# Performance work log

Measured on AMD Instinct MI355X. Metric: run time of the kernel, lower is better.

Reference implementation:

```python
import jax, jax.numpy as jnp
import numpy as np

AMPLITUDE_STD = 4.2  # repo constant (unexported); normalization scale for ln_mag
EPS = 1e-8


def _interp_bias(table, x):
    # Linear interpolation of a 1D table over frequency domain [-1, 1].
    n = table.shape[0]
    idx = jnp.clip((x + 1.0) * 0.5 * (n - 1), 0.0, float(n - 1))
    i0 = jnp.floor(idx).astype(jnp.int32)
    i1 = jnp.minimum(i0 + 1, n - 1)
    w = idx - i0.astype(idx.dtype)
    return table[i0] * (1.0 - w) + table[i1] * w


def setup_inputs() -> dict:
    key = jax.random.key(0)
    k1, k2, k3, k4 = jax.random.split(key, 4)
    B, F, P, W, H = 8, 128, 32, 96, 96
    return {
        "mode_shapes": jax.random.normal(k1, (B, 2, P, W, H), dtype=jnp.float32),
        "mode_responses": jax.random.normal(k2, (B, F, 2, P), dtype=jnp.float32),
        "freqs": jax.random.uniform(k3, (B, F), dtype=jnp.float32, minval=-1.0, maxval=1.0),
        "bias_table": jax.random.normal(k4, (250,), dtype=jnp.float32) * 0.1,
    }


def reference(mode_shapes, mode_responses, freqs, bias_table):
    B, _, P, W, H = mode_shapes.shape
    F = mode_responses.shape[1]
    # _normalize_mode: L2 norm over (real/imag, W, H) per (batch, peak)
    norm = jnp.sqrt(jnp.sum(mode_shapes ** 2, axis=(1, 3, 4)))  # (B,P)
    ms = mode_shapes / (norm[:, None, :, None, None] + EPS)
    s_r, s_i = ms[:, 0], ms[:, 1]                                # (B,P,W,H)
    t_r, t_i = mode_responses[:, :, 0], mode_responses[:, :, 1]  # (B,F,P)
    f = 1.0 / P
    # complex superposition over modes: contraction over n_peaks
    rr = jnp.einsum('bpwh,bfp->bfwh', s_r, t_r)
    ii = jnp.einsum('bpwh,bfp->bfwh', s_i, t_i)
    ri = jnp.einsum('bpwh,bfp->bfwh', s_r, t_i)
    ir = jnp.einsum('bpwh,bfp->bfwh', s_i, t_r)
    r_new = f * (rr - ii)  # (B,F,W,H)
    i_new = f * (ri + ir)
    mag2 = r_new ** 2 + i_new ** 2
    bias = _interp_bias(bias_table, freqs)                       # (B,F)
    ln_mag = (jnp.log(mag2 + EPS) + bias[:, :, None, None]) / AMPLITUDE_STD
    fnorm = jnp.sum(mag2, axis=(-1, -2), keepdims=True)
    fnorm = jnp.sqrt(jnp.clip(fnorm, jnp.finfo(fnorm.dtype).eps))
    normed_field = jnp.stack([r_new / fnorm, i_new / fnorm], axis=2)  # (B,F,2,W,H)
    # aux sparsity loss over mode responses
    mr = mode_responses.reshape(B, F * 2, P)
    aux_sparse = jnp.mean(jnp.mean(jnp.log(jnp.linalg.norm(mr, axis=1) + 1.0), axis=1))
    return ln_mag, normed_field, aux_sparse
```

## Files before the change

### kernel.cpp

```cpp
#include <hip/hip_runtime.h>
#include <math.h>

#define WHN 9216
#define PN 32
#define FN 128
#define BN 8
#define EPSF 1e-8f
#define INV_STD 0.23809523809f
#define AUX_IDX 28311552

typedef __attribute__((ext_vector_type(8))) short short8;
typedef __attribute__((ext_vector_type(16))) float f32x16;

__device__ __forceinline__ unsigned short f2bf(float x) {
  unsigned int u = __float_as_uint(x);
  unsigned int r = (u + 0x7FFFu + ((u >> 16) & 1u)) >> 16;
  return (unsigned short)r;
}
__device__ __forceinline__ float bf2f(unsigned short h) {
  return __uint_as_float(((unsigned int)h) << 16);
}

__global__ __launch_bounds__(256) void k_gram(const float* __restrict__ ms,
                                              float* __restrict__ wsM,
                                              float* __restrict__ wsA,
                                              float* __restrict__ part,
                                              int use_part) {
  const int b = blockIdx.y;
  const int chunk = blockIdx.x;
  const int tid = threadIdx.x;
  __shared__ float4 sA[32][32];
  __shared__ float4 sB[32][32];
  __shared__ float pbuf[2][2048];
  const float4* ms4 = (const float4*)ms;
#pragma unroll
  for (int k = 0; k < 4; ++k) {
    int i4 = tid + k * 256;
    int xq = i4 & 31, p = i4 >> 5;
    sA[xq][p ^ xq] = ms4[((b * 2 + 0) * 32 + p) * 2304 + chunk * 32 + xq];
    sB[xq][p ^ xq] = ms4[((b * 2 + 1) * 32 + p) * 2304 + chunk * 32 + xq];
  }
  __syncthreads();
  const int w = tid >> 6, lane = tid & 63;
  const int pg = lane & 7, qg = lane >> 3;
  float accM[4][4] = {{0}}, accA[4][4] = {{0}};
  for (int xq = w; xq < 32; xq += 4) {
    float4 pa[4], pb[4], qa[4], qb[4];
#pragma unroll
    for (int j = 0; j < 4; ++j) {
      pa[j] = sA[xq][(pg + 8 * j) ^ xq];
      pb[j] = sB[xq][(pg + 8 * j) ^ xq];
      qa[j] = sA[xq][(qg + 8 * j) ^ xq];
      qb[j] = sB[xq][(qg + 8 * j) ^ xq];
    }
#pragma unroll
    for (int j = 0; j < 4; ++j)
#pragma unroll
      for (int k = 0; k < 4; ++k) {
        accM[j][k] += pa[j].x * qa[k].x + pb[j].x * qb[k].x
                    + pa[j].y * qa[k].y + pb[j].y * qb[k].y
                    + pa[j].z * qa[k].z + pb[j].z * qb[k].z
                    + pa[j].w * qa[k].w + pb[j].w * qb[k].w;
        accA[j][k] += pa[j].x * qb[k].x - pb[j].x * qa[k].x
                    + pa[j].y * qb[k].y - pb[j].y * qa[k].y
                    + pa[j].z * qb[k].z - pb[j].z * qa[k].z
                    + pa[j].w * qb[k].w - pb[j].w * qa[k].w;
      }
  }
  if (w < 2) {
#pragma unroll
    for (int j = 0; j < 4; ++j)
#pragma unroll
      for (int k = 0; k < 4; ++k) {
        pbuf[w][lane * 32 + j * 4 + k] = accM[j][k];
        pbuf[w][lane * 32 + 16 + j * 4 + k] = accA[j][k];
      }
  }
  __syncthreads();
  if (w >= 2) {
#pragma unroll
    for (int j = 0; j < 4; ++j)
#pragma unroll
      for (int k = 0; k < 4; ++k) {
        pbuf[w - 2][lane * 32 + j * 4 + k] += accM[j][k];
        pbuf[w - 2][lane * 32 + 16 + j * 4 + k] += accA[j][k];
      }
  }
  __syncthreads();
  for (int idx = tid; idx < 2048; idx += 256) {
    float v = pbuf[0][idx] + pbuf[1][idx];
    if (use_part) {
      part[((size_t)(b * 72 + chunk)) * 2048 + idx] = v;
    } else {
      int lane2 = idx >> 5, r = idx & 31;
      int mat = r >> 4, rr = r & 15, j = rr >> 2, k = rr & 3;
      int p = (lane2 & 7) + 8 * j, q = (lane2 >> 3) + 8 * k;
      float* dst = mat ? wsA : wsM;
      atomicAdd(dst + (b << 10) + p * 32 + q, v);
    }
  }
}

__global__ __launch_bounds__(256) void k_mid(const float* __restrict__ part,
                                             float* __restrict__ wsM,
                                             float* __restrict__ wsA,
                                             float* __restrict__ wsc,
                                             float* __restrict__ out) {
  int g = blockIdx.x * 256 + threadIdx.x;
  if (g == 0) out[AUX_IDX] = 0.f;
  int b = g >> 11, idx = g & 2047;
  const float* p = part + ((size_t)b * 72) * 2048 + idx;
  float s = 0.f;
#pragma unroll 8
  for (int c = 0; c < 72; ++c) s += p[(size_t)c * 2048];
  int lane2 = idx >> 5, r = idx & 31;
  int mat = r >> 4, rr = r & 15, j = rr >> 2, k = rr & 3;
  int pp = (lane2 & 7) + 8 * j, q = (lane2 >> 3) + 8 * k;
  (mat ? wsA : wsM)[(b << 10) + pp * 32 + q] = s;
  if (!mat && pp == q) wsc[(b << 5) + pp] = (1.0f / 32.0f) / (sqrtf(s) + EPSF);
}

__global__ void k_cfromM(const float* __restrict__ wsM, float* __restrict__ wsc,
                         float* __restrict__ out) {
  int tid = threadIdx.x;
  if (tid == 0) out[AUX_IDX] = 0.f;
  int b = tid >> 5, p = tid & 31;
  float m = wsM[(b << 10) + p * 33];
  wsc[tid] = (1.0f / 32.0f) / (sqrtf(m) + EPSF);
}

__global__ __launch_bounds__(64) void k_fnb(const float* __restrict__ t,
                                            const float* __restrict__ freqs,
                                            const float* __restrict__ btab,
                                            const float* __restrict__ wsM,
                                            const float* __restrict__ wsA,
                                            const float* __restrict__ wsc,
                                            float* __restrict__ wsinv,
                                            float* __restrict__ wsbias,
                                            float* __restrict__ out) {
  const int lane = threadIdx.x;
  if (blockIdx.x >= 1024) {
    const int b = blockIdx.x - 1024;
    const int p = lane & 31, comp = lane >> 5;
    float acc = 0.f;
#pragma unroll 4
    for (int f = 0; f < FN; ++f) {
      float v = t[((size_t)(b * FN + f) * 2 + comp) * PN + p];
      acc = fmaf(v, v, acc);
    }
    acc += __shfl_xor(acc, 32);
    float val = logf(sqrtf(acc) + 1.0f);
#pragma unroll
    for (int off = 1; off <= 16; off <<= 1) val += __shfl_xor(val, off);
    if (lane == 0) atomicAdd(out + AUX_IDX, val * (1.0f / 256.0f));
    return;
  }
  const int bf = blockIdx.x;
  const int b = bf >> 7;
  __shared__ float tt[64];
  {
    int p = lane & 31, comp = lane >> 5;
    tt[lane] = t[(bf * 2 + comp) * PN + p] * wsc[(b << 5) + p];
  }
  __syncthreads();
  const int pp = lane & 31, qh = lane >> 5;
  const float* Mrow = wsM + (b << 10) + pp * 32 + qh * 16;
  const float* Arow = wsA + (b << 10) + pp * 32 + qh * 16;
  float ap = tt[pp], bp = tt[32 + pp];
  float S = 0.f;
#pragma unroll
  for (int k = 0; k < 16; ++k) {
    int q = qh * 16 + k;
    float aq = tt[q], bq = tt[32 + q];
    S += (ap * aq + bp * bq) * Mrow[k] + 2.0f * (bp * aq) * Arow[k];
  }
#pragma unroll
  for (int off = 32; off; off >>= 1) S += __shfl_xor(S, off);
  if (lane == 0) {
    float fn = sqrtf(fmaxf(S, 1.1920929e-7f));
    wsinv[bf] = 1.0f / fn;
    float x = freqs[bf];
    float idx = (x + 1.0f) * 0.5f * 249.0f;
    idx = fminf(fmaxf(idx, 0.0f), 249.0f);
    float fi = floorf(idx);
    int i0 = (int)fi;
    int i1 = min(i0 + 1, 249);
    float wvv = idx - fi;
    wsbias[bf] = btab[i0] * (1.0f - wvv) + btab[i1] * wvv;
  }
}

#define MFMA32(A, B, C) __builtin_amdgcn_mfma_f32_32x32x16_bf16(A, B, C, 0, 0, 0)
__global__ __launch_bounds__(256) void k_main(const float* __restrict__ ms,
                                              const float* __restrict__ t,
                                              const float* __restrict__ wsc,
                                              const float* __restrict__ wsinv,
                                              const float* __restrict__ wsbias,
                                              float* __restrict__ out) {
  __shared__ short tHs[4096];
  __shared__ short tLs[4096];
  __shared__ float sInv[64], sBias[64], sC[32];
  const int b = blockIdx.y;
  const int tid = threadIdx.x;
  const int lane = tid & 63, wv = tid >> 6;
  const int col = lane & 31, hf = lane >> 5;
  const int pix = blockIdx.x * 128 + wv * 32 + col;
  const int f0 = blockIdx.z * 64;

  const float* msb = ms + (size_t)b * 64 * WHN + pix;
  short8 sHf[4], sLf[4];
#pragma unroll
  for (int kg = 0; kg < 4; ++kg) {
#pragma unroll
    for (int j = 0; j < 8; ++j) {
      int k = kg * 16 + hf * 8 + j;
      float v = msb[(size_t)k * WHN];
      unsigned short h = f2bf(v);
      sHf[kg][j] = (short)h;
      sLf[kg][j] = (short)f2bf(v - bf2f(h));
    }
  }
  short8 msk;
#pragma unroll
  for (int j = 0; j < 8; ++j) msk[j] = (short)0x8000;
  short8 nH2 = sHf[2] ^ msk, nL2 = sLf[2] ^ msk;
  short8 nH3 = sHf[3] ^ msk, nL3 = sLf[3] ^ msk;

  if (tid < 64) sInv[tid] = wsinv[b * 128 + f0 + tid];
  else if (tid < 128) sBias[tid - 64] = wsbias[b * 128 + f0 + (tid - 64)];
  if (tid >= 224) sC[tid - 224] = wsc[b * 32 + (tid - 224)];
  __syncthreads();

#pragma unroll
  for (int it = 0; it < 2; ++it) {
    int gidx = tid + it * 256;
    int fl = gidx >> 3, g = gidx & 7;
    const float* src = t + ((size_t)(b * 128 + f0 + fl) * 2 + (g >> 2)) * 32 + (g & 3) * 8;
    int gs = g ^ (fl & 7);
    short8 hv, lv;
#pragma unroll
    for (int e = 0; e < 8; ++e) {
      float v = src[e] * sC[(g & 3) * 8 + e];
      unsigned short h = f2bf(v);
      hv[e] = (short)h;
      lv[e] = (short)f2bf(v - bf2f(h));
    }
    *(short8*)&tHs[fl * 64 + gs * 8] = hv;
    *(short8*)&tLs[fl * 64 + gs * 8] = lv;
  }
  __syncthreads();

  float* outF = out + (size_t)BN * FN * WHN;

#pragma unroll
  for (int ft = 0; ft < 2; ++ft) {
    short8 tHf[4], tLf[4];
    int fl = ft * 32 + col;
    int fx = fl & 7;
#pragma unroll
    for (int kg = 0; kg < 4; ++kg) {
      int gs = (2 * kg + hf) ^ fx;
      tHf[kg] = *(const short8*)&tHs[fl * 64 + gs * 8];
      tLf[kg] = *(const short8*)&tLs[fl * 64 + gs * 8];
    }
    f32x16 aR, aI;
#pragma unroll
    for (int i = 0; i < 16; ++i) { aR[i] = 0.f; aI[i] = 0.f; }
    aR = MFMA32(tHf[0], sHf[0], aR); aR = MFMA32(tHf[0], sLf[0], aR); aR = MFMA32(tLf[0], sHf[0], aR);
    aR = MFMA32(tHf[1], sHf[1], aR); aR = MFMA32(tHf[1], sLf[1], aR); aR = MFMA32(tLf[1], sHf[1], aR);
    aR = MFMA32(tHf[2], nH2,    aR); aR = MFMA32(tHf[2], nL2,    aR); aR = MFMA32(tLf[2], nH2,    aR);
    aR = MFMA32(tHf[3], nH3,    aR); aR = MFMA32(tHf[3], nL3,    aR); aR = MFMA32(tLf[3], nH3,    aR);
    aI = MFMA32(tHf[0], sHf[2], aI); aI = MFMA32(tHf[0], sLf[2], aI); aI = MFMA32(tLf[0], sHf[2], aI);
    aI = MFMA32(tHf[1], sHf[3], aI); aI = MFMA32(tHf[1], sLf[3], aI); aI = MFMA32(tLf[1], sHf[3], aI);
    aI = MFMA32(tHf[2], sHf[0], aI); aI = MFMA32(tHf[2], sLf[0], aI); aI = MFMA32(tLf[2], sHf[0], aI);
    aI = MFMA32(tHf[3], sHf[1], aI); aI = MFMA32(tHf[3], sLf[1], aI); aI = MFMA32(tLf[3], sHf[1], aI);
#pragma unroll
    for (int r = 0; r < 16; ++r) {
      int row = (r & 3) + 8 * (r >> 2) + 4 * hf;
      int fo = ft * 32 + row;
      float vr = aR[r], vi = aI[r];
      float mag2 = fmaf(vr, vr, vi * vi);
      float ln = (__logf(mag2 + EPSF) + sBias[fo]) * INV_STD;
      float inv = sInv[fo];
      size_t fg = (size_t)(b * 128 + f0 + fo);
      __builtin_nontemporal_store(ln, out + fg * WHN + pix);
      __builtin_nontemporal_store(vr * inv, outF + (fg * 2) * WHN + pix);
      __builtin_nontemporal_store(vi * inv, outF + (fg * 2 + 1) * WHN + pix);
    }
  }
}

extern "C" void kernel_launch(void* const* d_in, const int* in_sizes, int n_in,
                              void* d_out, int out_size, void* d_ws, size_t ws_size,
                              hipStream_t stream) {
  const float* ms = (const float*)d_in[0];
  const float* t  = (const float*)d_in[1];
  const float* fr = (const float*)d_in[2];
  const float* bt = (const float*)d_in[3];
  float* out = (float*)d_out;
  float* ws = (float*)d_ws;
  float* wsM = ws;
  float* wsA = ws + 8192;
  float* wsc = ws + 16384;
  float* wsinv = ws + 16640;
  float* wsbias = ws + 17664;
  float* part = ws + 18688;
  size_t need = ((size_t)18688 + (size_t)576 * 2048) * 4;
  int use_part = (ws_size >= need) ? 1 : 0;

  if (use_part) {
    hipLaunchKernelGGL(k_gram, dim3(72, 8), dim3(256), 0, stream, ms, wsM, wsA, part, 1);
    hipLaunchKernelGGL(k_mid, dim3(64), dim3(256), 0, stream, part, wsM, wsA, wsc, out);
  } else {
    hipMemsetAsync(ws, 0, 16384 * sizeof(float), stream);
    hipLaunchKernelGGL(k_gram, dim3(72, 8), dim3(256), 0, stream, ms, wsM, wsA, part, 0);
    hipLaunchKernelGGL(k_cfromM, dim3(1), dim3(256), 0, stream, wsM, wsc, out);
  }
  hipLaunchKernelGGL(k_fnb, dim3(1032), dim3(64), 0, stream, t, fr, bt, wsM, wsA, wsc, wsinv, wsbias, out);
  hipLaunchKernelGGL(k_main, dim3(72, 8, 2), dim3(256), 0, stream, ms, t, wsc, wsinv, wsbias, out);
}
```

Before: 171.6 us.

## Precompute split-bf16 mode-response tiles once and DMA them into LDS

The scaled, swizzled hi/lo bf16 split of the mode responses was recomputed by every k_main block (72x redundancy per batch/f-tile). Extra blocks in k_fnb now compute it once per batch into a workspace buffer. k_main loads it straight into LDS with global_load_lds, which removes per-block conversion work and one barrier. k_main also gains a min-blocks launch bound of 2 and uses the library bf16 conversion. The risks are extra workspace traffic and register pressure from the tighter launch bound.

```diff
diff --git a/kernel.cpp b/kernel.cpp
--- a/kernel.cpp
+++ b/kernel.cpp
@@ -1,4 +1,5 @@
 #include <hip/hip_runtime.h>
+#include <hip/hip_bf16.h>
 #include <math.h>
 
 #define WHN 9216
@@ -12,13 +13,16 @@
 typedef __attribute__((ext_vector_type(8))) short short8;
 typedef __attribute__((ext_vector_type(16))) float f32x16;
 
-__device__ __forceinline__ unsigned short f2bf(float x) {
-  unsigned int u = __float_as_uint(x);
-  unsigned int r = (u + 0x7FFFu + ((u >> 16) & 1u)) >> 16;
-  return (unsigned short)r;
-}
-__device__ __forceinline__ float bf2f(unsigned short h) {
-  return __uint_as_float(((unsigned int)h) << 16);
+__device__ __forceinline__ unsigned short bfbits(__hip_bfloat16 h) {
+  return *reinterpret_cast<unsigned short*>(&h);
+}
+
+__device__ __forceinline__ unsigned int bfsplit_pk(float v) {
+  __hip_bfloat16 h = __float2bfloat16(v);
+  unsigned int hs = bfbits(h);
+  float r = v - __bfloat162float(h);
+  unsigned int ls = bfbits(__float2bfloat16(r));
+  return hs | (ls << 16);
 }
 
 __global__ __launch_bounds__(256) void k_gram(const float* __restrict__ ms,
@@ -137,8 +141,34 @@
                                             const float* __restrict__ wsc,
                                             float* __restrict__ wsinv,
                                             float* __restrict__ wsbias,
+                                            short* __restrict__ wsT,
                                             float* __restrict__ out) {
   const int lane = threadIdx.x;
+  if (blockIdx.x >= 1032) {
+    const int b = blockIdx.x - 1032;
+    __shared__ float sc[32];
+    if (lane < 32) sc[lane] = wsc[b * 32 + lane];
+    __syncthreads();
+    short* dstH = wsT + (size_t)b * 16384;
+    short* dstL = dstH + 8192;
+#pragma unroll 2
+    for (int it = 0; it < 16; ++it) {
+      int slot = it * 64 + lane;
+      int fl = slot >> 3, g = slot & 7;
+      const float* src = t + ((size_t)(b * 128 + fl) * 2 + (g >> 2)) * 32 + (g & 3) * 8;
+      int gs = g ^ (fl & 7);
+      short8 hv, lv;
+#pragma unroll
+      for (int e = 0; e < 8; ++e) {
+        unsigned int pk = bfsplit_pk(src[e] * sc[(g & 3) * 8 + e]);
+        hv[e] = (short)(pk & 0xFFFFu);
+        lv[e] = (short)(pk >> 16);
+      }
+      *(short8*)&dstH[fl * 64 + gs * 8] = hv;
+      *(short8*)&dstL[fl * 64 + gs * 8] = lv;
+    }
+    return;
+  }
   if (blockIdx.x >= 1024) {
     const int b = blockIdx.x - 1024;
     const int p = lane & 31, comp = lane >> 5;
@@ -191,21 +221,36 @@
 }
 
 #define MFMA32(A, B, C) __builtin_amdgcn_mfma_f32_32x32x16_bf16(A, B, C, 0, 0, 0)
-__global__ __launch_bounds__(256) void k_main(const float* __restrict__ ms,
-                                              const float* __restrict__ t,
-                                              const float* __restrict__ wsc,
-                                              const float* __restrict__ wsinv,
-                                              const float* __restrict__ wsbias,
-                                              float* __restrict__ out) {
+__global__ __launch_bounds__(256, 2) void k_main(const float* __restrict__ ms,
+                                                 const short* __restrict__ wsT,
+                                                 const float* __restrict__ wsinv,
+                                                 const float* __restrict__ wsbias,
+                                                 float* __restrict__ out) {
   __shared__ short tHs[4096];
   __shared__ short tLs[4096];
-  __shared__ float sInv[64], sBias[64], sC[32];
+  __shared__ float sInv[64], sBias[64];
   const int b = blockIdx.y;
+  const int z = blockIdx.z;
   const int tid = threadIdx.x;
   const int lane = tid & 63, wv = tid >> 6;
   const int col = lane & 31, hf = lane >> 5;
   const int pix = blockIdx.x * 128 + wv * 32 + col;
-  const int f0 = blockIdx.z * 64;
+  const int f0 = z * 64;
+
+  {
+    const short* gH = wsT + (size_t)b * 16384 + (size_t)z * 4096;
+#pragma unroll
+    for (int it = 0; it < 4; ++it) {
+      int chunk = wv * 4 + it;
+      int half = chunk >> 3;
+      int off = (chunk & 7) * 512;
+      const short* g = gH + half * 8192 + off + lane * 8;
+      short* l = (half ? tLs : tHs) + off;
+      __builtin_amdgcn_global_load_lds(
+          (const __attribute__((address_space(1))) unsigned int*)g,
+          (__attribute__((address_space(3))) unsigned int*)l, 16, 0, 0);
+    }
+  }
 
   const float* msb = ms + (size_t)b * 64 * WHN + pix;
   short8 sHf[4], sLf[4];
@@ -214,10 +259,9 @@
 #pragma unroll
     for (int j = 0; j < 8; ++j) {
       int k = kg * 16 + hf * 8 + j;
-      float v = msb[(size_t)k * WHN];
-      unsigned short h = f2bf(v);
-      sHf[kg][j] = (short)h;
-      sLf[kg][j] = (short)f2bf(v - bf2f(h));
+      unsigned int pk = bfsplit_pk(msb[(size_t)k * WHN]);
+      sHf[kg][j] = (short)(pk & 0xFFFFu);
+      sLf[kg][j] = (short)(pk >> 16);
     }
   }
   short8 msk;
@@ -228,26 +272,6 @@
 
   if (tid < 64) sInv[tid] = wsinv[b * 128 + f0 + tid];
   else if (tid < 128) sBias[tid - 64] = wsbias[b * 128 + f0 + (tid - 64)];
-  if (tid >= 224) sC[tid - 224] = wsc[b * 32 + (tid - 224)];
-  __syncthreads();
-
-#pragma unroll
-  for (int it = 0; it < 2; ++it) {
-    int gidx = tid + it * 256;
-    int fl = gidx >> 3, g = gidx & 7;
-    const float* src = t + ((size_t)(b * 128 + f0 + fl) * 2 + (g >> 2)) * 32 + (g & 3) * 8;
-    int gs = g ^ (fl & 7);
-    short8 hv, lv;
-#pragma unroll
-    for (int e = 0; e < 8; ++e) {
-      float v = src[e] * sC[(g & 3) * 8 + e];
-      unsigned short h = f2bf(v);
-      hv[e] = (short)h;
-      lv[e] = (short)f2bf(v - bf2f(h));
-    }
-    *(short8*)&tHs[fl * 64 + gs * 8] = hv;
-    *(short8*)&tLs[fl * 64 + gs * 8] = lv;
-  }
   __syncthreads();
 
   float* outF = out + (size_t)BN * FN * WHN;
@@ -305,17 +329,19 @@
   float* wsinv = ws + 16640;
   float* wsbias = ws + 17664;
   float* part = ws + 18688;
-  size_t need = ((size_t)18688 + (size_t)576 * 2048) * 4;
+  const size_t PART_FLOATS = (size_t)576 * 2048;
+  size_t need = ((size_t)18688 + PART_FLOATS + 65536) * 4;
   int use_part = (ws_size >= need) ? 1 : 0;
+  short* wsT = use_part ? (short*)(part + PART_FLOATS) : (short*)(ws + 18688);
 
   if (use_part) {
     hipLaunchKernelGGL(k_gram, dim3(72, 8), dim3(256), 0, stream, ms, wsM, wsA, part, 1);
     hipLaunchKernelGGL(k_mid, dim3(64), dim3(256), 0, stream, part, wsM, wsA, wsc, out);
   } else {
-    hipMemsetAsync(ws, 0, 16384 * sizeof(float), stream);
+    (void)hipMemsetAsync(ws, 0, 16384 * sizeof(float), stream);
     hipLaunchKernelGGL(k_gram, dim3(72, 8), dim3(256), 0, stream, ms, wsM, wsA, part, 0);
     hipLaunchKernelGGL(k_cfromM, dim3(1), dim3(256), 0, stream, wsM, wsc, out);
   }
-  hipLaunchKernelGGL(k_fnb, dim3(1032), dim3(64), 0, stream, t, fr, bt, wsM, wsA, wsc, wsinv, wsbias, out);
-  hipLaunchKernelGGL(k_main, dim3(72, 8, 2), dim3(256), 0, stream, ms, t, wsc, wsinv, wsbias, out);
-}
+  hipLaunchKernelGGL(k_fnb, dim3(1040), dim3(64), 0, stream, t, fr, bt, wsM, wsA, wsc, wsinv, wsbias, wsT, out);
+  hipLaunchKernelGGL(k_main, dim3(72, 8, 2), dim3(256), 0, stream, ms, wsT, wsinv, wsbias, out);
+}
```

New measurement: 167.2 us. 1.03x faster.
